# Performance work log

Measured on AMD Instinct MI355X. Metric: run time of the kernel, lower is better.

## Reference

```python
import jax, jax.numpy as jnp
import numpy as np

ALPHA = 0.1
B = 500_000
EMBED = 64
HIDDEN = 128
IN_DIM = 27 + 3 + EMBED  # 94

def _gelu(x):
    return jax.nn.gelu(x, approximate=False)  # torch.nn.GELU default = exact erf

def setup_inputs() -> dict:
    key = jax.random.key(0)
    ks = jax.random.split(key, 8)
    s = 0.05
    return {
        "F": jnp.eye(3, dtype=jnp.float32)[None] + 0.1 * jax.random.normal(ks[0], (B, 3, 3), jnp.float32),
        "latent_weight": jax.random.normal(ks[1], (1024, EMBED), jnp.float32),
        "W1": s * jax.random.normal(ks[2], (IN_DIM, HIDDEN), jnp.float32), "b1": jnp.zeros((HIDDEN,), jnp.float32),
        "W2": s * jax.random.normal(ks[3], (HIDDEN, HIDDEN), jnp.float32), "b2": jnp.zeros((HIDDEN,), jnp.float32),
        "W3": s * jax.random.normal(ks[4], (HIDDEN, HIDDEN), jnp.float32), "b3": jnp.zeros((HIDDEN,), jnp.float32),
        "W4": s * jax.random.normal(ks[5], (HIDDEN, HIDDEN), jnp.float32), "b4": jnp.zeros((HIDDEN,), jnp.float32),
        "W5": s * jax.random.normal(ks[6], (HIDDEN, 9), jnp.float32), "b5": jnp.zeros((9,), jnp.float32),
        "traj_ids": jnp.asarray(7, dtype=jnp.int32),
    }

def reference(F, latent_weight, W1, b1, W2, b2, W3, b3, W4, b4, W5, b5, traj_ids):
    n = F.shape[0]
    # Batched 3x3 SVD: F = U diag(s) Vh  (torch.svd returns V; Vh = V^T here)
    U, sigma, Vh = jnp.linalg.svd(F, full_matrices=False)
    R = jnp.matmul(U, Vh)  # [n,3,3] rotation
    lat = jnp.broadcast_to(latent_weight[traj_ids][None, :], (n, latent_weight.shape[1]))
    inv = jnp.concatenate(
        [F.reshape(n, 9), U.reshape(n, 9), sigma, Vh.reshape(n, 9), lat], axis=1)  # [n, 30+embed]
    h = _gelu(inv @ W1 + b1)
    h = _gelu(h @ W2 + b2)
    h = _gelu(h @ W3 + b3)
    h = _gelu(h @ W4 + b4)
    x = (h @ W5 + b5).reshape(n, 3, 3)
    x = 0.5 * (x + jnp.swapaxes(x, 1, 2))  # symmetrize
    return ALPHA * jnp.matmul(R, x) + F
```

## Files before the change

kernel.cpp:

```cpp
#include <hip/hip_runtime.h>


typedef short bf16x8 __attribute__((ext_vector_type(8)));
typedef short bf16x4 __attribute__((ext_vector_type(4)));
typedef float f32x4 __attribute__((ext_vector_type(4)));
typedef unsigned short u16;

#define WS_L1     0
#define WS_L234   8192
#define WS_L5     106496
#define WS_B1EFF  110592
#define WS_B234   111104
#define WS_B5     112640
#define WS_NEEDED 131072

__device__ __forceinline__ float bf2f(u16 b){
  union { unsigned int u; float f; } v; v.u = ((unsigned int)b) << 16; return v.f;
}
__device__ __forceinline__ u16 f2bf(float f){
  union { float f; unsigned int u; } v; v.f = f;
  unsigned int x = v.u;
  return (u16)((x + 0x7fffu + ((x >> 16) & 1u)) >> 16);
}
template<bool B16>
__device__ __forceinline__ float ldf(const void* p, int i){
  return B16 ? bf2f(((const u16*)p)[i]) : ((const float*)p)[i];
}
template<bool B16>
__device__ __forceinline__ short ldw(const void* p, int i){
  return B16 ? (short)((const u16*)p)[i] : (short)f2bf(((const float*)p)[i]);
}
template<bool B16>
__device__ __forceinline__ void stf(void* p, int i, float v){
  if (B16) ((u16*)p)[i] = f2bf(v); else ((float*)p)[i] = v;
}

__device__ __forceinline__ float gelu_f(float x){
  float s = x * x;
  float z = x * __builtin_fmaf(-0.10294329f, s, -2.3022082f);
#if __has_builtin(__builtin_amdgcn_exp2f)
  float e = __builtin_amdgcn_exp2f(z);
#else
  float e = __expf(0.6931471806f * z);
#endif
#if __has_builtin(__builtin_amdgcn_rcpf)
  return x * __builtin_amdgcn_rcpf(1.0f + e);
#else
  return x / (1.0f + e);
#endif
}

__device__ __forceinline__ int sniff_bf16(const void* Fg){
  const u16* fu = (const u16*)Fg;
  int votes = 0;
  #pragma unroll
  for (int k = 0; k < 32; ++k){
    u16 h = fu[k*18];
    votes += (h >= 0x3E00 && h < 0x4000) ? 1 : 0;
  }
  return votes >= 16;
}

template<int P, int Q, int R3>
__device__ __forceinline__ void jrot(float bm[3][3], float v[3][3]){
  float bpq = bm[P][Q];
  if (fabsf(bpq) < 1e-30f) return;
  float th = (bm[Q][Q] - bm[P][P]) / (2.0f * bpq);
  float t = copysignf(1.0f, th) / (fabsf(th) + sqrtf(1.0f + th*th));
  float c = 1.0f / sqrtf(1.0f + t*t);
  float s = t * c;
  float bpp = bm[P][P] - t*bpq;
  float bqq = bm[Q][Q] + t*bpq;
  bm[P][P] = bpp; bm[Q][Q] = bqq; bm[P][Q] = 0.0f; bm[Q][P] = 0.0f;
  float bpr = bm[P][R3], bqr = bm[Q][R3];
  float npr = c*bpr - s*bqr;
  float nqr = s*bpr + c*bqr;
  bm[P][R3] = npr; bm[R3][P] = npr;
  bm[Q][R3] = nqr; bm[R3][Q] = nqr;
  #pragma unroll
  for (int i = 0; i < 3; ++i){
    float vp = v[i][P], vq = v[i][Q];
    v[i][P] = c*vp - s*vq;
    v[i][Q] = s*vp + c*vq;
  }
}

__device__ __forceinline__ void svd3(const float Fm[9],
                                     float u[3][3], float sg[3], float vt[3][3]){
  float bm[3][3];
  #pragma unroll
  for (int i = 0; i < 3; ++i)
    #pragma unroll
    for (int j = i; j < 3; ++j){
      float acc = Fm[0*3+i]*Fm[0*3+j] + Fm[1*3+i]*Fm[1*3+j] + Fm[2*3+i]*Fm[2*3+j];
      bm[i][j] = acc; bm[j][i] = acc;
    }
  float v[3][3] = {{1.f,0.f,0.f},{0.f,1.f,0.f},{0.f,0.f,1.f}};
  #pragma unroll
  for (int sweep = 0; sweep < 6; ++sweep){
    jrot<0,1,2>(bm, v);
    jrot<0,2,1>(bm, v);
    jrot<1,2,0>(bm, v);
  }
  float lam0 = bm[0][0], lam1 = bm[1][1], lam2 = bm[2][2];
  #define CSWAP(la, lb, A, Bc) if ((la) < (lb)) { float t_ = la; la = lb; lb = t_; \
    for (int i_ = 0; i_ < 3; ++i_){ float w_ = v[i_][A]; v[i_][A] = v[i_][Bc]; v[i_][Bc] = w_; } }
  CSWAP(lam0, lam1, 0, 1);
  CSWAP(lam0, lam2, 0, 2);
  CSWAP(lam1, lam2, 1, 2);
  #undef CSWAP
  float a[3][3];
  #pragma unroll
  for (int c = 0; c < 3; ++c)
    #pragma unroll
    for (int r = 0; r < 3; ++r)
      a[r][c] = Fm[r*3+0]*v[0][c] + Fm[r*3+1]*v[1][c] + Fm[r*3+2]*v[2][c];
  float s1 = sqrtf(a[0][0]*a[0][0] + a[1][0]*a[1][0] + a[2][0]*a[2][0]);
  float inv1 = 1.0f / fmaxf(s1, 1e-30f);
  u[0][0] = a[0][0]*inv1; u[1][0] = a[1][0]*inv1; u[2][0] = a[2][0]*inv1;
  float d12 = u[0][0]*a[0][1] + u[1][0]*a[1][1] + u[2][0]*a[2][1];
  float w20 = a[0][1] - d12*u[0][0], w21 = a[1][1] - d12*u[1][0], w22 = a[2][1] - d12*u[2][0];
  float s2 = sqrtf(w20*w20 + w21*w21 + w22*w22);
  float inv2 = 1.0f / fmaxf(s2, 1e-30f);
  u[0][1] = w20*inv2; u[1][1] = w21*inv2; u[2][1] = w22*inv2;
  float d13 = u[0][0]*a[0][2] + u[1][0]*a[1][2] + u[2][0]*a[2][2];
  float d23 = u[0][1]*a[0][2] + u[1][1]*a[1][2] + u[2][1]*a[2][2];
  float w30 = a[0][2] - d13*u[0][0] - d23*u[0][1];
  float w31 = a[1][2] - d13*u[1][0] - d23*u[1][1];
  float w32 = a[2][2] - d13*u[2][0] - d23*u[2][1];
  float s3 = sqrtf(w30*w30 + w31*w31 + w32*w32);
  if (s3 > 1e-12f){
    float inv3 = 1.0f / s3;
    u[0][2] = w30*inv3; u[1][2] = w31*inv3; u[2][2] = w32*inv3;
  } else {
    float c0 = u[1][0]*u[2][1] - u[2][0]*u[1][1];
    float c1 = u[2][0]*u[0][1] - u[0][0]*u[2][1];
    float c2 = u[0][0]*u[1][1] - u[1][0]*u[0][1];
    float dt = c0*a[0][2] + c1*a[1][2] + c2*a[2][2];
    float sgn = (dt < 0.0f) ? -1.0f : 1.0f;
    u[0][2] = c0*sgn; u[1][2] = c1*sgn; u[2][2] = c2*sgn;
    s3 = fabsf(dt);
  }
  sg[0] = s1; sg[1] = s2; sg[2] = s3;
  #pragma unroll
  for (int i = 0; i < 3; ++i)
    #pragma unroll
    for (int j = 0; j < 3; ++j)
      vt[i][j] = v[j][i];
}

template<bool B16>
__device__ void prep_body(
  const void* latg, const void* w1g, const void* b1g,
  const void* w2g, const void* b2g, const void* w3g, const void* b3g,
  const void* w4g, const void* b4g, const void* w5g, const void* b5g,
  const int* trajg, char* ws)
{
  const int tid = threadIdx.x, lane = tid & 63, wv = tid >> 6;
  const int quad = lane >> 4, l15 = lane & 15;
  const int blk = blockIdx.x;
  if (blk < 27){
    const int wr = blk*4 + wv;
    bf16x8 frag;
    if (wr < 8){
      const int ntg = wr;
      #pragma unroll
      for (int j = 0; j < 8; ++j)
        frag[j] = ldw<B16>(w1g, (quad*8 + j)*128 + ntg*16 + l15);
      *(bf16x8*)(ws + WS_L1 + (size_t)(wr*64 + lane)*16) = frag;
    } else if (wr < 104){
      const int idx = wr - 8, layer = idx >> 5, rem = idx & 31;
      const int ntg = rem >> 2, ks = rem & 3;
      const void* wg = (layer == 0) ? w2g : ((layer == 1) ? w3g : w4g);
      #pragma unroll
      for (int j = 0; j < 8; ++j)
        frag[j] = ldw<B16>(wg, (ks*32 + quad*8 + j)*128 + ntg*16 + l15);
      *(bf16x8*)(ws + WS_L234 + (size_t)(idx*64 + lane)*16) = frag;
    } else {
      const int ks = wr - 104;
      #pragma unroll
      for (int j = 0; j < 8; ++j)
        frag[j] = (l15 < 9) ? ldw<B16>(w5g, (ks*32 + quad*8 + j)*9 + l15) : (short)0;
      *(bf16x8*)(ws + WS_L5 + (size_t)(ks*64 + lane)*16) = frag;
    }
  } else {
    if (tid < 128){
      const int t7 = trajg[0];
      float acc = ldf<B16>(b1g, tid);
      for (int j = 0; j < 64; ++j)
        acc += ldf<B16>(latg, t7*64 + j) * ldf<B16>(w1g, (30 + j)*128 + tid);
      ((float*)(ws + WS_B1EFF))[tid] = acc;
    } else {
      const int n = tid - 128;
      ((float*)(ws + WS_B234))[0*128 + n] = ldf<B16>(b2g, n);
      ((float*)(ws + WS_B234))[1*128 + n] = ldf<B16>(b3g, n);
      ((float*)(ws + WS_B234))[2*128 + n] = ldf<B16>(b4g, n);
      if (n < 16) ((float*)(ws + WS_B5))[n] = (n < 9) ? ldf<B16>(b5g, n) : 0.0f;
    }
  }
}

__global__ __launch_bounds__(256)
void fproj_prep_kernel(
  const void* Fg, const void* latg, const void* w1g, const void* b1g,
  const void* w2g, const void* b2g, const void* w3g, const void* b3g,
  const void* w4g, const void* b4g, const void* w5g, const void* b5g,
  const int* __restrict__ trajg, char* ws)
{
  if (sniff_bf16(Fg))
    prep_body<true >(latg, w1g, b1g, w2g, b2g, w3g, b3g, w4g, b4g, w5g, b5g, trajg, ws);
  else
    prep_body<false>(latg, w1g, b1g, w2g, b2g, w3g, b3g, w4g, b4g, w5g, b5g, trajg, ws);
}

union ShA { u16 X0[128][40]; float Xout[128][16]; };

template<bool B16, bool WS>
__device__ __forceinline__ void mlp_layer128(
    u16 (&Hbuf)[128][136],
    const void* __restrict__ Wg, const void* __restrict__ bg,
    const char* __restrict__ wsW, const float* __restrict__ bf32,
    int wv, int lane)
{
  const int l15  = lane & 15;
  const int quad = lane >> 4;
  const int kb   = quad * 8;
  bf16x8 Wf[2][4];
  #pragma unroll
  for (int nt = 0; nt < 2; ++nt){
    const int ntg = wv*2 + nt;
    #pragma unroll
    for (int ks = 0; ks < 4; ++ks){
      if (WS){
        Wf[nt][ks] = *(const bf16x8*)(wsW + (size_t)((ntg*4 + ks)*64 + lane)*16);
      } else {
        bf16x8 bv;
        #pragma unroll
        for (int j = 0; j < 8; ++j)
          bv[j] = ldw<B16>(Wg, (ks*32 + kb + j)*128 + ntg*16 + l15);
        Wf[nt][ks] = bv;
      }
    }
  }
  f32x4 acc[8][2];
  #pragma unroll
  for (int mt = 0; mt < 8; ++mt){
    const u16* hp = &Hbuf[mt*16 + l15][kb];
    bf16x8 a0 = *(const bf16x8*)(hp);
    bf16x8 a1 = *(const bf16x8*)(hp + 32);
    bf16x8 a2 = *(const bf16x8*)(hp + 64);
    bf16x8 a3 = *(const bf16x8*)(hp + 96);
    #pragma unroll
    for (int nt = 0; nt < 2; ++nt){
      f32x4 c = {0.f,0.f,0.f,0.f};
      c = __builtin_amdgcn_mfma_f32_16x16x32_bf16(Wf[nt][0], a0, c, 0,0,0);
      c = __builtin_amdgcn_mfma_f32_16x16x32_bf16(Wf[nt][1], a1, c, 0,0,0);
      c = __builtin_amdgcn_mfma_f32_16x16x32_bf16(Wf[nt][2], a2, c, 0,0,0);
      c = __builtin_amdgcn_mfma_f32_16x16x32_bf16(Wf[nt][3], a3, c, 0,0,0);
      acc[mt][nt] = c;
    }
  }
  __syncthreads();
  #pragma unroll
  for (int nt = 0; nt < 2; ++nt){
    const int n0 = wv*32 + nt*16 + quad*4;
    f32x4 bb;
    if (WS) bb = *(const f32x4*)(bf32 + n0);
    else { bb[0]=ldf<B16>(bg,n0); bb[1]=ldf<B16>(bg,n0+1); bb[2]=ldf<B16>(bg,n0+2); bb[3]=ldf<B16>(bg,n0+3); }
    #pragma unroll
    for (int mt = 0; mt < 8; ++mt){
      f32x4 c = acc[mt][nt];
      bf16x4 pk;
      #pragma unroll
      for (int rg = 0; rg < 4; ++rg)
        pk[rg] = (short)f2bf(gelu_f(c[rg] + bb[rg]));
      *(bf16x4*)&Hbuf[mt*16 + l15][n0] = pk;
    }
  }
  __syncthreads();
}

template<bool B16, bool WS>
__device__ void fproj_body(
  const void* Fg, const void* latg,
  const void* w1g, const void* b1g, const void* w2g, const void* b2g,
  const void* w3g, const void* b3g, const void* w4g, const void* b4g,
  const void* w5g, const void* b5g,
  const int* trajg, void* outg, int ntot, const char* ws,
  ShA& shA, u16 (&Hbuf)[128][136], float (&b1lds)[128])
{
  const int tid  = threadIdx.x;
  const int lane = tid & 63;
  const int wv   = tid >> 6;
  const int l15  = lane & 15;
  const int quad = lane >> 4;
  const int kb   = quad * 8;
  const int row0 = blockIdx.x * 128;

  float Freg[9];
  float Rm[3][3];

  bf16x8 Wf1[2];
  #pragma unroll
  for (int nt = 0; nt < 2; ++nt){
    const int ntg = wv*2 + nt;
    if (WS){
      Wf1[nt] = *(const bf16x8*)(ws + WS_L1 + (size_t)(ntg*64 + lane)*16);
    } else {
      bf16x8 bv;
      #pragma unroll
      for (int j = 0; j < 8; ++j)
        bv[j] = ldw<B16>(w1g, (kb + j)*128 + ntg*16 + l15);
      Wf1[nt] = bv;
    }
  }

  if (tid < 128){
    const int r = row0 + tid;
    u16 feat[32];
    if (r < ntot){
      float A0[9];
      #pragma unroll
      for (int k = 0; k < 9; ++k){ A0[k] = ldf<B16>(Fg, r*9 + k); Freg[k] = A0[k]; }
      float uu[3][3], ss[3], vvt[3][3];
      svd3(A0, uu, ss, vvt);
      #pragma unroll
      for (int i = 0; i < 3; ++i)
        #pragma unroll
        for (int j = 0; j < 3; ++j)
          Rm[i][j] = uu[i][0]*vvt[0][j] + uu[i][1]*vvt[1][j] + uu[i][2]*vvt[2][j];
      #pragma unroll
      for (int k = 0; k < 9; ++k) feat[k]    = f2bf(A0[k]);
      #pragma unroll
      for (int k = 0; k < 9; ++k) feat[9+k]  = f2bf(uu[k/3][k%3]);
      feat[18] = f2bf(ss[0]); feat[19] = f2bf(ss[1]); feat[20] = f2bf(ss[2]);
      #pragma unroll
      for (int k = 0; k < 9; ++k) feat[21+k] = f2bf(vvt[k/3][k%3]);
      feat[30] = 0; feat[31] = 0;
    } else {
      #pragma unroll
      for (int k = 0; k < 32; ++k) feat[k] = 0;
      #pragma unroll
      for (int k = 0; k < 9; ++k) Freg[k] = 0.0f;
      #pragma unroll
      for (int i = 0; i < 3; ++i)
        #pragma unroll
        for (int j = 0; j < 3; ++j) Rm[i][j] = 0.0f;
    }
    #pragma unroll
    for (int p = 0; p < 4; ++p){
      bf16x8 pk;
      #pragma unroll
      for (int j = 0; j < 8; ++j) pk[j] = (short)feat[p*8 + j];
      *(bf16x8*)&shA.X0[tid][p*8] = pk;
    }
  } else if (!WS){
    const int n = tid - 128;
    const int t7 = trajg[0];
    float acc = ldf<B16>(b1g, n);
    for (int j = 0; j < 64; ++j)
      acc += ldf<B16>(latg, t7*64 + j) * ldf<B16>(w1g, (30 + j)*128 + n);
    b1lds[n] = acc;
  }
  __syncthreads();

  {
    f32x4 acc[8][2];
    #pragma unroll
    for (int mt = 0; mt < 8; ++mt){
      bf16x8 av = *(const bf16x8*)&shA.X0[mt*16 + l15][kb];
      #pragma unroll
      for (int nt = 0; nt < 2; ++nt){
        f32x4 c = {0.f,0.f,0.f,0.f};
        c = __builtin_amdgcn_mfma_f32_16x16x32_bf16(Wf1[nt], av, c, 0,0,0);
        acc[mt][nt] = c;
      }
    }
    __syncthreads();
    #pragma unroll
    for (int nt = 0; nt < 2; ++nt){
      const int n0 = wv*32 + nt*16 + quad*4;
      f32x4 bb;
      if (WS) bb = *(const f32x4*)((const float*)(ws + WS_B1EFF) + n0);
      else { bb[0]=b1lds[n0]; bb[1]=b1lds[n0+1]; bb[2]=b1lds[n0+2]; bb[3]=b1lds[n0+3]; }
      #pragma unroll
      for (int mt = 0; mt < 8; ++mt){
        f32x4 c = acc[mt][nt];
        bf16x4 pk;
        #pragma unroll
        for (int rg = 0; rg < 4; ++rg)
          pk[rg] = (short)f2bf(gelu_f(c[rg] + bb[rg]));
        *(bf16x4*)&Hbuf[mt*16 + l15][n0] = pk;
      }
    }
  }
  __syncthreads();

  const float* bf32 = (const float*)(ws + WS_B234);
  mlp_layer128<B16,WS>(Hbuf, w2g, b2g, ws + WS_L234 + 0*32768, bf32 + 0*128, wv, lane);
  mlp_layer128<B16,WS>(Hbuf, w3g, b3g, ws + WS_L234 + 1*32768, bf32 + 1*128, wv, lane);
  mlp_layer128<B16,WS>(Hbuf, w4g, b4g, ws + WS_L234 + 2*32768, bf32 + 2*128, wv, lane);

  {
    bf16x8 W5f[4];
    #pragma unroll
    for (int ks = 0; ks < 4; ++ks){
      if (WS){
        W5f[ks] = *(const bf16x8*)(ws + WS_L5 + (size_t)(ks*64 + lane)*16);
      } else {
        bf16x8 bv;
        #pragma unroll
        for (int j = 0; j < 8; ++j)
          bv[j] = (l15 < 9) ? ldw<B16>(w5g, (ks*32 + kb + j)*9 + l15) : (short)0;
        W5f[ks] = bv;
      }
    }
    f32x4 bb5;
    if (WS) bb5 = *(const f32x4*)((const float*)(ws + WS_B5) + quad*4);
    else {
      #pragma unroll
      for (int rg = 0; rg < 4; ++rg)
        bb5[rg] = (quad*4 + rg < 9) ? ldf<B16>(b5g, quad*4 + rg) : 0.0f;
    }
    #pragma unroll
    for (int t = 0; t < 2; ++t){
      const int mt = wv*2 + t;
      const u16* hp = &Hbuf[mt*16 + l15][kb];
      bf16x8 a0 = *(const bf16x8*)(hp);
      bf16x8 a1 = *(const bf16x8*)(hp + 32);
      bf16x8 a2 = *(const bf16x8*)(hp + 64);
      bf16x8 a3 = *(const bf16x8*)(hp + 96);
      f32x4 c = {0.f,0.f,0.f,0.f};
      c = __builtin_amdgcn_mfma_f32_16x16x32_bf16(W5f[0], a0, c, 0,0,0);
      c = __builtin_amdgcn_mfma_f32_16x16x32_bf16(W5f[1], a1, c, 0,0,0);
      c = __builtin_amdgcn_mfma_f32_16x16x32_bf16(W5f[2], a2, c, 0,0,0);
      c = __builtin_amdgcn_mfma_f32_16x16x32_bf16(W5f[3], a3, c, 0,0,0);
      c += bb5;
      *(f32x4*)&shA.Xout[mt*16 + l15][quad*4] = c;
    }
  }
  __syncthreads();

  if (tid < 128){
    const int r = row0 + tid;
    if (r < ntot){
      float x[9];
      #pragma unroll
      for (int k = 0; k < 9; ++k) x[k] = shA.Xout[tid][k];
      float xs[3][3];
      #pragma unroll
      for (int i = 0; i < 3; ++i)
        #pragma unroll
        for (int j = 0; j < 3; ++j)
          xs[i][j] = 0.5f*(x[i*3+j] + x[j*3+i]);
      #pragma unroll
      for (int i = 0; i < 3; ++i)
        #pragma unroll
        for (int j = 0; j < 3; ++j){
          float y = Rm[i][0]*xs[0][j] + Rm[i][1]*xs[1][j] + Rm[i][2]*xs[2][j];
          stf<B16>(outg, r*9 + i*3 + j, 0.1f*y + Freg[i*3+j]);
        }
    }
  }
}

__global__ __launch_bounds__(256, 3)
void fproj_ws_kernel(
  const void* Fg, const void* latg,
  const void* w1g, const void* b1g, const void* w2g, const void* b2g,
  const void* w3g, const void* b3g, const void* w4g, const void* b4g,
  const void* w5g, const void* b5g,
  const int* __restrict__ trajg, void* outg, int ntot, const char* ws)
{
  __shared__ ShA shA;
  __shared__ alignas(16) u16 Hbuf[128][136];
  __shared__ float b1lds[128];
  if (sniff_bf16(Fg))
    fproj_body<true , true>(Fg, latg, w1g, b1g, w2g, b2g, w3g, b3g, w4g, b4g,
                            w5g, b5g, trajg, outg, ntot, ws, shA, Hbuf, b1lds);
  else
    fproj_body<false, true>(Fg, latg, w1g, b1g, w2g, b2g, w3g, b3g, w4g, b4g,
                            w5g, b5g, trajg, outg, ntot, ws, shA, Hbuf, b1lds);
}

__global__ __launch_bounds__(256, 3)
void fproj_plain_kernel(
  const void* Fg, const void* latg,
  const void* w1g, const void* b1g, const void* w2g, const void* b2g,
  const void* w3g, const void* b3g, const void* w4g, const void* b4g,
  const void* w5g, const void* b5g,
  const int* __restrict__ trajg, void* outg, int ntot)
{
  __shared__ ShA shA;
  __shared__ alignas(16) u16 Hbuf[128][136];
  __shared__ float b1lds[128];
  if (sniff_bf16(Fg))
    fproj_body<true , false>(Fg, latg, w1g, b1g, w2g, b2g, w3g, b3g, w4g, b4g,
                             w5g, b5g, trajg, outg, ntot, nullptr, shA, Hbuf, b1lds);
  else
    fproj_body<false, false>(Fg, latg, w1g, b1g, w2g, b2g, w3g, b3g, w4g, b4g,
                             w5g, b5g, trajg, outg, ntot, nullptr, shA, Hbuf, b1lds);
}

extern "C" void kernel_launch(void* const* d_in, const int* in_sizes, int n_in,
                              void* d_out, int out_size, void* d_ws, size_t ws_size,
                              hipStream_t stream) {
  (void)n_in; (void)out_size;
  const int n = in_sizes[0] / 9;
  dim3 grid((n + 127) / 128), block(256);
  if (ws_size >= (size_t)WS_NEEDED){
    hipLaunchKernelGGL(fproj_prep_kernel, dim3(28), block, 0, stream,
      (const void*)d_in[0],  (const void*)d_in[1],
      (const void*)d_in[2],  (const void*)d_in[3],
      (const void*)d_in[4],  (const void*)d_in[5],
      (const void*)d_in[6],  (const void*)d_in[7],
      (const void*)d_in[8],  (const void*)d_in[9],
      (const void*)d_in[10], (const void*)d_in[11],
      (const int*)d_in[12], (char*)d_ws);
    hipLaunchKernelGGL(fproj_ws_kernel, grid, block, 0, stream,
      (const void*)d_in[0],  (const void*)d_in[1],
      (const void*)d_in[2],  (const void*)d_in[3],
      (const void*)d_in[4],  (const void*)d_in[5],
      (const void*)d_in[6],  (const void*)d_in[7],
      (const void*)d_in[8],  (const void*)d_in[9],
      (const void*)d_in[10], (const void*)d_in[11],
      (const int*)d_in[12], d_out, n, (const char*)d_ws);
  } else {
    hipLaunchKernelGGL(fproj_plain_kernel, grid, block, 0, stream,
      (const void*)d_in[0],  (const void*)d_in[1],
      (const void*)d_in[2],  (const void*)d_in[3],
      (const void*)d_in[4],  (const void*)d_in[5],
      (const void*)d_in[6],  (const void*)d_in[7],
      (const void*)d_in[8],  (const void*)d_in[9],
      (const void*)d_in[10], (const void*)d_in[11],
      (const int*)d_in[12], d_out, n);
  }
}
```

Before: 232.8 us.

## Use polynomial GELU, fold bias into MFMA accumulators, pack bf16 pairs, fewer Jacobi sweeps

Replaces the exp/rcp-based GELU with a clamped odd polynomial evaluated with med3 and FMAs. Bias vectors now initialise the MFMA accumulators instead of being added in the epilogue. Float-to-bf16 conversion packs two values per perm instruction. The Jacobi SVD drops from six to five sweeps, and the unused b1 LDS array is removed from the workspace kernel. The aim is to cut VALU/transcendental work in the epilogues and the SVD, at the cost of GELU approximation error and possibly less converged SVD results.

Measured after the change: 210.9 us. 9.4% less time.

```diff
diff --git a/kernel.cpp b/kernel.cpp
--- a/kernel.cpp
+++ b/kernel.cpp
@@ -4,6 +4,7 @@
 typedef short bf16x8 __attribute__((ext_vector_type(8)));
 typedef short bf16x4 __attribute__((ext_vector_type(4)));
 typedef float f32x4 __attribute__((ext_vector_type(4)));
+typedef unsigned int u32x2 __attribute__((ext_vector_type(2)));
 typedef unsigned short u16;
 
 #define WS_L1     0
@@ -22,6 +23,16 @@
   unsigned int x = v.u;
   return (u16)((x + 0x7fffu + ((x >> 16) & 1u)) >> 16);
 }
+__device__ __forceinline__ unsigned int packbf2(float f0, float f1){
+  union { float f; unsigned int u; } a, b; a.f = f0; b.f = f1;
+  unsigned int u0 = a.u + 0x7fffu + ((a.u >> 16) & 1u);
+  unsigned int u1 = b.u + 0x7fffu + ((b.u >> 16) & 1u);
+#if __has_builtin(__builtin_amdgcn_perm)
+  return __builtin_amdgcn_perm(u1, u0, 0x07060302u);
+#else
+  return (u0 >> 16) | (u1 & 0xffff0000u);
+#endif
+}
 template<bool B16>
 __device__ __forceinline__ float ldf(const void* p, int i){
   return B16 ? bf2f(((const u16*)p)[i]) : ((const float*)p)[i];
@@ -35,19 +46,22 @@
   if (B16) ((u16*)p)[i] = f2bf(v); else ((float*)p)[i] = v;
 }
 
+__device__ __forceinline__ float med3f(float x, float lo, float hi){
+#if __has_builtin(__builtin_amdgcn_fmed3f)
+  return __builtin_amdgcn_fmed3f(x, lo, hi);
+#else
+  return fminf(fmaxf(x, lo), hi);
+#endif
+}
+
 __device__ __forceinline__ float gelu_f(float x){
-  float s = x * x;
-  float z = x * __builtin_fmaf(-0.10294329f, s, -2.3022082f);
-#if __has_builtin(__builtin_amdgcn_exp2f)
-  float e = __builtin_amdgcn_exp2f(z);
-#else
-  float e = __expf(0.6931471806f * z);
-#endif
-#if __has_builtin(__builtin_amdgcn_rcpf)
-  return x * __builtin_amdgcn_rcpf(1.0f + e);
-#else
-  return x / (1.0f + e);
-#endif
+  float xc = med3f(x, -3.4f, 3.4f);
+  float s  = xc * xc;
+  float g  = __builtin_fmaf(s, __builtin_fmaf(s,
+               __builtin_fmaf(s, -2.20713e-4f, 5.86695e-3f),
+               -5.99485e-2f), 3.969014e-1f);
+  float ph = med3f(__builtin_fmaf(xc, g, 0.5f), 0.0f, 1.0f);
+  return x * ph;
 }
 
 __device__ __forceinline__ int sniff_bf16(const void* Fg){
@@ -97,7 +111,7 @@
     }
   float v[3][3] = {{1.f,0.f,0.f},{0.f,1.f,0.f},{0.f,0.f,1.f}};
   #pragma unroll
-  for (int sweep = 0; sweep < 6; ++sweep){
+  for (int sweep = 0; sweep < 5; ++sweep){
     jrot<0,1,2>(bm, v);
     jrot<0,2,1>(bm, v);
     jrot<1,2,0>(bm, v);
@@ -225,6 +239,14 @@
   const int l15  = lane & 15;
   const int quad = lane >> 4;
   const int kb   = quad * 8;
+  f32x4 bb[2];
+  #pragma unroll
+  for (int nt = 0; nt < 2; ++nt){
+    const int n0 = wv*32 + nt*16 + quad*4;
+    if (WS) bb[nt] = *(const f32x4*)(bf32 + n0);
+    else { bb[nt][0]=ldf<B16>(bg,n0); bb[nt][1]=ldf<B16>(bg,n0+1);
+           bb[nt][2]=ldf<B16>(bg,n0+2); bb[nt][3]=ldf<B16>(bg,n0+3); }
+  }
   bf16x8 Wf[2][4];
   #pragma unroll
   for (int nt = 0; nt < 2; ++nt){
@@ -252,7 +274,7 @@
     bf16x8 a3 = *(const bf16x8*)(hp + 96);
     #pragma unroll
     for (int nt = 0; nt < 2; ++nt){
-      f32x4 c = {0.f,0.f,0.f,0.f};
+      f32x4 c = bb[nt];
       c = __builtin_amdgcn_mfma_f32_16x16x32_bf16(Wf[nt][0], a0, c, 0,0,0);
       c = __builtin_amdgcn_mfma_f32_16x16x32_bf16(Wf[nt][1], a1, c, 0,0,0);
       c = __builtin_amdgcn_mfma_f32_16x16x32_bf16(Wf[nt][2], a2, c, 0,0,0);
@@ -264,17 +286,13 @@
   #pragma unroll
   for (int nt = 0; nt < 2; ++nt){
     const int n0 = wv*32 + nt*16 + quad*4;
-    f32x4 bb;
-    if (WS) bb = *(const f32x4*)(bf32 + n0);
-    else { bb[0]=ldf<B16>(bg,n0); bb[1]=ldf<B16>(bg,n0+1); bb[2]=ldf<B16>(bg,n0+2); bb[3]=ldf<B16>(bg,n0+3); }
     #pragma unroll
     for (int mt = 0; mt < 8; ++mt){
       f32x4 c = acc[mt][nt];
-      bf16x4 pk;
-      #pragma unroll
-      for (int rg = 0; rg < 4; ++rg)
-        pk[rg] = (short)f2bf(gelu_f(c[rg] + bb[rg]));
-      *(bf16x4*)&Hbuf[mt*16 + l15][n0] = pk;
+      u32x2 pk;
+      pk[0] = packbf2(gelu_f(c[0]), gelu_f(c[1]));
+      pk[1] = packbf2(gelu_f(c[2]), gelu_f(c[3]));
+      *(u32x2*)&Hbuf[mt*16 + l15][n0] = pk;
     }
   }
   __syncthreads();
@@ -287,7 +305,7 @@
   const void* w3g, const void* b3g, const void* w4g, const void* b4g,
   const void* w5g, const void* b5g,
   const int* trajg, void* outg, int ntot, const char* ws,
-  ShA& shA, u16 (&Hbuf)[128][136], float (&b1lds)[128])
+  ShA& shA, u16 (&Hbuf)[128][136], float* b1lds)
 {
   const int tid  = threadIdx.x;
   const int lane = tid & 63;
@@ -317,7 +335,7 @@
 
   if (tid < 128){
     const int r = row0 + tid;
-    u16 feat[32];
+    float fv[32];
     if (r < ntot){
       float A0[9];
       #pragma unroll
@@ -330,16 +348,16 @@
         for (int j = 0; j < 3; ++j)
           Rm[i][j] = uu[i][0]*vvt[0][j] + uu[i][1]*vvt[1][j] + uu[i][2]*vvt[2][j];
       #pragma unroll
-      for (int k = 0; k < 9; ++k) feat[k]    = f2bf(A0[k]);
-      #pragma unroll
-      for (int k = 0; k < 9; ++k) feat[9+k]  = f2bf(uu[k/3][k%3]);
-      feat[18] = f2bf(ss[0]); feat[19] = f2bf(ss[1]); feat[20] = f2bf(ss[2]);
-      #pragma unroll
-      for (int k = 0; k < 9; ++k) feat[21+k] = f2bf(vvt[k/3][k%3]);
-      feat[30] = 0; feat[31] = 0;
+      for (int k = 0; k < 9; ++k) fv[k]    = A0[k];
+      #pragma unroll
+      for (int k = 0; k < 9; ++k) fv[9+k]  = uu[k/3][k%3];
+      fv[18] = ss[0]; fv[19] = ss[1]; fv[20] = ss[2];
+      #pragma unroll
+      for (int k = 0; k < 9; ++k) fv[21+k] = vvt[k/3][k%3];
+      fv[30] = 0.0f; fv[31] = 0.0f;
     } else {
       #pragma unroll
-      for (int k = 0; k < 32; ++k) feat[k] = 0;
+      for (int k = 0; k < 32; ++k) fv[k] = 0.0f;
       #pragma unroll
       for (int k = 0; k < 9; ++k) Freg[k] = 0.0f;
       #pragma unroll
@@ -348,11 +366,22 @@
         for (int j = 0; j < 3; ++j) Rm[i][j] = 0.0f;
     }
     #pragma unroll
-    for (int p = 0; p < 4; ++p){
-      bf16x8 pk;
-      #pragma unroll
-      for (int j = 0; j < 8; ++j) pk[j] = (short)feat[p*8 + j];
-      *(bf16x8*)&shA.X0[tid][p*8] = pk;
+    for (int p = 0; p < 2; ++p){
+      f32x4 dummy;
+      u32x2 pk0, pk1;
+      pk0[0] = packbf2(fv[p*16+0],  fv[p*16+1]);
+      pk0[1] = packbf2(fv[p*16+2],  fv[p*16+3]);
+      pk1[0] = packbf2(fv[p*16+4],  fv[p*16+5]);
+      pk1[1] = packbf2(fv[p*16+6],  fv[p*16+7]);
+      *(u32x2*)&shA.X0[tid][p*16 + 0] = pk0;
+      *(u32x2*)&shA.X0[tid][p*16 + 4] = pk1;
+      pk0[0] = packbf2(fv[p*16+8],  fv[p*16+9]);
+      pk0[1] = packbf2(fv[p*16+10], fv[p*16+11]);
+      pk1[0] = packbf2(fv[p*16+12], fv[p*16+13]);
+      pk1[1] = packbf2(fv[p*16+14], fv[p*16+15]);
+      *(u32x2*)&shA.X0[tid][p*16 + 8]  = pk0;
+      *(u32x2*)&shA.X0[tid][p*16 + 12] = pk1;
+      (void)dummy;
     }
   } else if (!WS){
     const int n = tid - 128;
@@ -365,13 +394,20 @@
   __syncthreads();
 
   {
+    f32x4 bb[2];
+    #pragma unroll
+    for (int nt = 0; nt < 2; ++nt){
+      const int n0 = wv*32 + nt*16 + quad*4;
+      if (WS) bb[nt] = *(const f32x4*)((const float*)(ws + WS_B1EFF) + n0);
+      else { bb[nt][0]=b1lds[n0]; bb[nt][1]=b1lds[n0+1]; bb[nt][2]=b1lds[n0+2]; bb[nt][3]=b1lds[n0+3]; }
+    }
     f32x4 acc[8][2];
     #pragma unroll
     for (int mt = 0; mt < 8; ++mt){
       bf16x8 av = *(const bf16x8*)&shA.X0[mt*16 + l15][kb];
       #pragma unroll
       for (int nt = 0; nt < 2; ++nt){
-        f32x4 c = {0.f,0.f,0.f,0.f};
+        f32x4 c = bb[nt];
         c = __builtin_amdgcn_mfma_f32_16x16x32_bf16(Wf1[nt], av, c, 0,0,0);
         acc[mt][nt] = c;
       }
@@ -380,17 +416,13 @@
     #pragma unroll
     for (int nt = 0; nt < 2; ++nt){
       const int n0 = wv*32 + nt*16 + quad*4;
-      f32x4 bb;
-      if (WS) bb = *(const f32x4*)((const float*)(ws + WS_B1EFF) + n0);
-      else { bb[0]=b1lds[n0]; bb[1]=b1lds[n0+1]; bb[2]=b1lds[n0+2]; bb[3]=b1lds[n0+3]; }
       #pragma unroll
       for (int mt = 0; mt < 8; ++mt){
         f32x4 c = acc[mt][nt];
-        bf16x4 pk;
-        #pragma unroll
-        for (int rg = 0; rg < 4; ++rg)
-          pk[rg] = (short)f2bf(gelu_f(c[rg] + bb[rg]));
-        *(bf16x4*)&Hbuf[mt*16 + l15][n0] = pk;
+        u32x2 pk;
+        pk[0] = packbf2(gelu_f(c[0]), gelu_f(c[1]));
+        pk[1] = packbf2(gelu_f(c[2]), gelu_f(c[3]));
+        *(u32x2*)&Hbuf[mt*16 + l15][n0] = pk;
       }
     }
   }
@@ -430,12 +462,11 @@
       bf16x8 a1 = *(const bf16x8*)(hp + 32);
       bf16x8 a2 = *(const bf16x8*)(hp + 64);
       bf16x8 a3 = *(const bf16x8*)(hp + 96);
-      f32x4 c = {0.f,0.f,0.f,0.f};
+      f32x4 c = bb5;
       c = __builtin_amdgcn_mfma_f32_16x16x32_bf16(W5f[0], a0, c, 0,0,0);
       c = __builtin_amdgcn_mfma_f32_16x16x32_bf16(W5f[1], a1, c, 0,0,0);
       c = __builtin_amdgcn_mfma_f32_16x16x32_bf16(W5f[2], a2, c, 0,0,0);
       c = __builtin_amdgcn_mfma_f32_16x16x32_bf16(W5f[3], a3, c, 0,0,0);
-      c += bb5;
       *(f32x4*)&shA.Xout[mt*16 + l15][quad*4] = c;
     }
   }
@@ -474,13 +505,12 @@
 {
   __shared__ ShA shA;
   __shared__ alignas(16) u16 Hbuf[128][136];
-  __shared__ float b1lds[128];
   if (sniff_bf16(Fg))
     fproj_body<true , true>(Fg, latg, w1g, b1g, w2g, b2g, w3g, b3g, w4g, b4g,
-                            w5g, b5g, trajg, outg, ntot, ws, shA, Hbuf, b1lds);
+                            w5g, b5g, trajg, outg, ntot, ws, shA, Hbuf, nullptr);
   else
     fproj_body<false, true>(Fg, latg, w1g, b1g, w2g, b2g, w3g, b3g, w4g, b4g,
-                            w5g, b5g, trajg, outg, ntot, ws, shA, Hbuf, b1lds);
+                            w5g, b5g, trajg, outg, ntot, ws, shA, Hbuf, nullptr);
 }
 
 __global__ __launch_bounds__(256, 3)
```
